# Performance work log

Measured on AMD Instinct MI355X. Metric: run time of the kernel, lower is better.

The kernel has to match this reference:

```python
import jax, jax.numpy as jnp
import numpy as np

ROI_SIZE = 7
MAX_BIN_H = 8   # max adaptive-maxpool bin height for crop H <= 37
MAX_BIN_W = 9   # max adaptive-maxpool bin width  for crop W <= 50
SCALE = 0.0625  # 1/16 feature stride


def setup_inputs() -> dict:
    key = jax.random.key(0)
    ks = jax.random.split(key, 12)
    B, C, h, w = 1, 512, 37, 50          # conv5 feature map of a 600x800 image
    N = 512                               # number of ROIs (proposals)
    n_class = 21
    d_in, d_fc = C * ROI_SIZE * ROI_SIZE, 4096
    x = jax.random.normal(ks[0], (B, C, h, w), dtype=jnp.float32)
    # rois in image coordinates (x1, y1, x2, y2), image is 800x600
    x1 = jax.random.uniform(ks[1], (N,), minval=0.0, maxval=700.0)
    y1 = jax.random.uniform(ks[2], (N,), minval=0.0, maxval=500.0)
    bw = jax.random.uniform(ks[3], (N,), minval=16.0, maxval=400.0)
    bh = jax.random.uniform(ks[4], (N,), minval=16.0, maxval=300.0)
    rois = jnp.stack([x1, y1, jnp.minimum(x1 + bw, 799.0), jnp.minimum(y1 + bh, 599.0)], axis=1).astype(jnp.float32)
    roi_index = jnp.zeros((N,), dtype=jnp.int32)  # single image in batch
    W1 = jax.random.normal(ks[5], (d_in, d_fc), dtype=jnp.float32) * 0.01
    b1 = jnp.zeros((d_fc,), dtype=jnp.float32)
    W2 = jax.random.normal(ks[6], (d_fc, d_fc), dtype=jnp.float32) * 0.01
    b2 = jnp.zeros((d_fc,), dtype=jnp.float32)
    Wp = jax.random.normal(ks[7], (d_fc, n_class * 4), dtype=jnp.float32) * 0.001
    bp = jax.random.normal(ks[8], (n_class * 4,), dtype=jnp.float32) * 0.001
    Ws = jax.random.normal(ks[9], (d_fc, n_class), dtype=jnp.float32) * 0.01
    bs = jax.random.normal(ks[10], (n_class,), dtype=jnp.float32) * 0.01
    return dict(x=x, rois=rois, roi_index=roi_index, W1=W1, b1=b1, W2=W2, b2=b2, Wp=Wp, bp=bp, Ws=Ws, bs=bs)


def _roi_pool(x, rois, roi_index):
    """Faithful port of roi_pooling(): per-ROI crop + AdaptiveMaxPool2d(7)."""
    B, C, h, w = x.shape
    S = ROI_SIZE
    coords = jnp.round(rois * SCALE)  # round-half-even, like torch.round
    cx1 = jnp.clip(coords[:, 0], 0, w).astype(jnp.int32)
    cy1 = jnp.clip(coords[:, 1], 0, h).astype(jnp.int32)
    cx2 = jnp.clip(coords[:, 2], 0, w).astype(jnp.int32)
    cy2 = jnp.clip(coords[:, 3], 0, h).astype(jnp.int32)
    bidx = roi_index.astype(jnp.int32)
    roi_stack = jnp.stack([bidx, cx1, cy1, cx2, cy2], axis=1)  # [N,5]

    def pool_one(carry, roi):
        bi, x1i, y1i, x2i, y2i = roi[0], roi[1], roi[2], roi[3], roi[4]
        valid = (x1i < x2i) & (y1i < y2i)
        # torch slicing roi[2]:roi[4]+1 silently truncates at the tensor edge
        x2e = jnp.minimum(x2i, w - 1)
        y2e = jnp.minimum(y2i, h - 1)
        Hc = y2e - y1i + 1
        Wc = x2e - x1i + 1
        i = jnp.arange(S)
        # adaptive max pool bins: [floor(i*H/S), ceil((i+1)*H/S))
        rs = y1i + (i * Hc) // S
        re = y1i + ((i + 1) * Hc + S - 1) // S
        cs = x1i + (i * Wc) // S
        ce = x1i + ((i + 1) * Wc + S - 1) // S
        rows = rs[:, None] + jnp.arange(MAX_BIN_H)          # [S, MBH]
        rmask = rows < re[:, None]
        rows = jnp.clip(rows, 0, h - 1)
        cols = cs[:, None] + jnp.arange(MAX_BIN_W)          # [S, MBW]
        cmask = cols < ce[:, None]
        cols = jnp.clip(cols, 0, w - 1)
        feat = x[bi]                                         # [C, h, w]
        g = feat[:, rows[:, None, :, None], cols[None, :, None, :]]  # [C,S,S,MBH,MBW]
        mask = rmask[:, None, :, None] & cmask[None, :, None, :]     # [S,S,MBH,MBW]
        pooled = jnp.where(mask, g, -jnp.inf).max(axis=(-2, -1))    # [C,S,S]
        pooled = jnp.where(valid, pooled, jnp.zeros_like(pooled))
        return carry, pooled

    _, out = jax.lax.scan(pool_one, None, roi_stack)  # [N, C, S, S]
    return out


def reference(x, rois, roi_index, W1, b1, W2, b2, Wp, bp, Ws, bs):
    pooled = _roi_pool(x, rois, roi_index)            # [N, 512, 7, 7]
    flat = pooled.reshape(pooled.shape[0], -1)        # [N, 25088]
    fc6 = jax.nn.relu(flat @ W1 + b1)                 # [N, 4096]
    fc7 = jax.nn.relu(fc6 @ W2 + b2)                  # [N, 4096]
    roi_class_params = fc7 @ Wp + bp                  # [N, n_class*4]
    roi_scores = fc7 @ Ws + bs                        # [N, n_class]
    return (roi_class_params, roi_scores)
```

## Files before the change

### kernel.cpp

```cpp
#include <hip/hip_runtime.h>
#include <hip/hip_bf16.h>

using f32x4  = float          __attribute__((ext_vector_type(4)));
using bf16x8 = __bf16         __attribute__((ext_vector_type(8)));
using u16x8  = unsigned short __attribute__((ext_vector_type(8)));

#define C_CH 512
#define H_IN 37
#define W_IN 50
#define NPOS 1850
#define NROI 512
#define DIN  25088
#define DFC  4096
#define NPAR 84
#define NCLS 21
#define KS1   4
#define KS2   8
#define KSH   8

#define PB_X  232
#define PB_WH 2048
#define PB_TOT (PB_X + PB_WH)

__device__ __forceinline__ unsigned pack_bf16x2(float a, float b) {
    __hip_bfloat162 h;
    h.x = __float2bfloat16(a);
    h.y = __float2bfloat16(b);
    return *reinterpret_cast<unsigned*>(&h);
}

__global__ __launch_bounds__(256) void prep_kernel(
        const float* __restrict__ x, float* __restrict__ xt,
        const float* __restrict__ Wp, const float* __restrict__ Ws,
        float* __restrict__ Whp) {
    __shared__ float tile[64][65];
    int b = blockIdx.x;
    int t = threadIdx.x;
    if (b < PB_X) {
        int p0 = (b % 29) * 64;
        int c0 = (b / 29) * 64;
        int tc = t & 63, tr = t >> 6;
#pragma unroll
        for (int i = 0; i < 16; ++i) {
            int r = tr + i * 4;
            int p = p0 + tc;
            float v = 0.f;
            if (p < NPOS) v = x[(size_t)(c0 + r) * NPOS + p];
            tile[r][tc] = v;
        }
        __syncthreads();
#pragma unroll
        for (int i = 0; i < 16; ++i) {
            int rw = tr + i * 4;
            int p = p0 + rw;
            if (p < NPOS) xt[(size_t)p * C_CH + c0 + tc] = tile[tc][rw];
        }
    } else {
        int idx = (b - PB_X) * 256 + t;
        int k = idx >> 7, c = idx & 127;
        float v = 0.f;
        if (c < NPAR) v = Wp[(size_t)k * NPAR + c];
        else if (c < NPAR + NCLS) v = Ws[(size_t)k * NCLS + (c - NPAR)];
        Whp[idx] = v;
    }
}

__global__ __launch_bounds__(256) void roi_pool_kernel(
        const float* __restrict__ xt, const float* __restrict__ rois,
        __hip_bfloat16* __restrict__ pooled) {
    int n = blockIdx.x;
    int t = threadIdx.x;
    float4 rv = reinterpret_cast<const float4*>(rois)[n];
    int x1 = (int)fminf(fmaxf(rintf(rv.x * 0.0625f), 0.f), (float)W_IN);
    int y1 = (int)fminf(fmaxf(rintf(rv.y * 0.0625f), 0.f), (float)H_IN);
    int x2 = (int)fminf(fmaxf(rintf(rv.z * 0.0625f), 0.f), (float)W_IN);
    int y2 = (int)fminf(fmaxf(rintf(rv.w * 0.0625f), 0.f), (float)H_IN);
    bool valid = (x1 < x2) && (y1 < y2);
    unsigned* outp = reinterpret_cast<unsigned*>(pooled) + (size_t)n * (DIN / 2);
    if (!valid) {
        for (int b = 0; b < 49; ++b) outp[b * 256 + t] = 0u;
        return;
    }
    int x2e = min(x2, W_IN - 1), y2e = min(y2, H_IN - 1);
    int Hc = y2e - y1 + 1, Wc = x2e - x1 + 1;
    const float2* base = reinterpret_cast<const float2*>(xt);
    for (int i = 0; i < 7; ++i) {
        int rs = y1 + (i * Hc) / 7;
        int re = y1 + ((i + 1) * Hc + 6) / 7;
        for (int j = 0; j < 7; ++j) {
            int cs = x1 + (j * Wc) / 7;
            int ce = x1 + ((j + 1) * Wc + 6) / 7;
            float m0 = -__builtin_inff(), m1 = -__builtin_inff();
            for (int r = rs; r < re; ++r) {
                const float2* rowp = base + (size_t)r * (W_IN * C_CH / 2) + t;
                for (int c = cs; c < ce; ++c) {
                    float2 v = rowp[c * (C_CH / 2)];
                    m0 = fmaxf(m0, v.x);
                    m1 = fmaxf(m1, v.y);
                }
            }
            outp[(i * 7 + j) * 256 + t] = pack_bf16x2(m0, m1);
        }
    }
}

__device__ __forceinline__ void gload_lds16(const void* src, void* dst) {
    __builtin_amdgcn_global_load_lds(
        (const __attribute__((address_space(1))) void*)src,
        (__attribute__((address_space(3))) void*)dst, 16, 0, 0);
}

__global__ __launch_bounds__(256, 2) void gemm_f32b_kernel(
        const __hip_bfloat16* __restrict__ A,
        const float* __restrict__ Bf,
        float* __restrict__ Cp,
        int N, int lda, int ldbn, int kChunk, int nMT, int nNT, int Mtot,
        int perm) {
    __shared__ __align__(16) char lA0[16384];
    __shared__ __align__(16) char lA1[16384];
    __shared__ __align__(16) char lA2[16384];
    __shared__ __align__(16) char lB0[16384];
    __shared__ __align__(16) char lB1[16384];

    int q = gridDim.x >> 3;
    int bid = (blockIdx.x & 7) * q + (blockIdx.x >> 3);
    int mt = bid % nMT;
    int nt = (bid / nMT) % nNT;
    int ks = bid / (nMT * nNT);
    int m0 = mt * 128, n0 = nt * 128;
    int k0 = ks * kChunk;
    int t = threadIdx.x;
    int lane = t & 63, wid = t >> 6;

    const char* srcA[4]; int offA[4];
#pragma unroll
    for (int i = 0; i < 4; ++i) {
        int chunk = i * 4 + wid;
        int p = chunk * 1024 + lane * 16;
        int row = p >> 7;
        int swz = ((row ^ (row >> 3)) & 7) << 4;
        srcA[i] = (const char*)A + ((size_t)(m0 + row) * lda + k0) * 2
                  + ((p & 127) ^ swz);
        offA[i] = chunk * 1024;
    }
    auto stageA = [&](char* buf) {
#pragma unroll
        for (int i = 0; i < 4; ++i) {
            gload_lds16(srcA[i], buf + offA[i]);
            srcA[i] += 128;
        }
    };

    int n4 = (t & 31) * 4;
    int k8 = (t >> 5) * 8;
    int rstr = perm ? 49 : 1;
    const float* pB = Bf + n0 + n4;
    int koff[8];
#pragma unroll
    for (int p = 0; p < 8; ++p) koff[p] = (k8 + p) * rstr * ldbn;
    int woff[4];
#pragma unroll
    for (int j = 0; j < 4; ++j) {
        int row = n4 + j;
        int swz = ((row ^ (row >> 3)) & 7) << 4;
        woff[j] = row * 128 + ((k8 * 2) ^ swz);
    }
    auto loadB = [&](int kt, f32x4 (&v)[8]) {
        int kb = k0 + (kt << 6);
        int rb = perm ? ((kb & 511) * 49 + (kb >> 9)) : kb;
        int rbo = rb * ldbn;
#pragma unroll
        for (int p = 0; p < 8; ++p)
            v[p] = *reinterpret_cast<const f32x4*>(pB + (size_t)(rbo + koff[p]));
    };
    auto cvtB = [&](f32x4 (&v)[8], char* bW) {
#pragma unroll
        for (int j = 0; j < 4; ++j) {
            uint4 w;
            w.x = pack_bf16x2(v[0][j], v[1][j]);
            w.y = pack_bf16x2(v[2][j], v[3][j]);
            w.z = pack_bf16x2(v[4][j], v[5][j]);
            w.w = pack_bf16x2(v[6][j], v[7][j]);
            *reinterpret_cast<uint4*>(bW + woff[j]) = w;
        }
    };

    int wm = wid >> 1, wn = wid & 1;
    int kb0 = (lane >> 4) << 4;
    int roA[4], roB[4], sA[4], sB[4];
#pragma unroll
    for (int f = 0; f < 4; ++f) {
        int ra = wm * 64 + f * 16 + (lane & 15);
        int rb = wn * 64 + f * 16 + (lane & 15);
        roA[f] = ra * 128; sA[f] = ((ra ^ (ra >> 3)) & 7) << 4;
        roB[f] = rb * 128; sB[f] = ((rb ^ (rb >> 3)) & 7) << 4;
    }

    f32x4 acc[4][4] = {};
    auto mfmaStep = [&](const char* bA, const char* bB) {
        __builtin_amdgcn_s_setprio(1);
#pragma unroll
        for (int ksub = 0; ksub < 2; ++ksub) {
            int kk = kb0 | (ksub << 6);
            bf16x8 af[4], bfr[4];
#pragma unroll
            for (int f = 0; f < 4; ++f)
                af[f] = *reinterpret_cast<const bf16x8*>(bA + roA[f] + (kk ^ sA[f]));
#pragma unroll
            for (int f = 0; f < 4; ++f)
                bfr[f] = *reinterpret_cast<const bf16x8*>(bB + roB[f] + (kk ^ sB[f]));
#pragma unroll
            for (int mf = 0; mf < 4; ++mf)
#pragma unroll
                for (int nf = 0; nf < 4; ++nf)
                    acc[mf][nf] = __builtin_amdgcn_mfma_f32_16x16x32_bf16(
                        af[mf], bfr[nf], acc[mf][nf], 0, 0, 0);
        }
        __builtin_amdgcn_s_setprio(0);
    };

    f32x4 sP[8], sQ[8];
    auto body = [&](int kt, char* aR, char* aS,
                    f32x4 (&vC)[8], f32x4 (&vL)[8], char* bR, char* bW) {
        stageA(aS);
        loadB(kt + 2, vL);
        mfmaStep(aR, bR);
        cvtB(vC, bW);
        asm volatile("s_waitcnt lgkmcnt(0)\ns_barrier" ::: "memory");
    };

    int nkt = kChunk >> 6;

    stageA(lA0);
    stageA(lA1);
    loadB(0, sP);
    loadB(1, sQ);
    cvtB(sP, lB0);
    asm volatile("s_waitcnt lgkmcnt(0)\ns_barrier" ::: "memory");

    for (int kt = 0; kt + 2 < nkt; kt += 6) {
        body(kt + 0, lA0, lA2, sQ, sP, lB0, lB1);
        body(kt + 1, lA1, lA0, sP, sQ, lB1, lB0);
        body(kt + 2, lA2, lA1, sQ, sP, lB0, lB1);
        body(kt + 3, lA0, lA2, sP, sQ, lB1, lB0);
        body(kt + 4, lA1, lA0, sQ, sP, lB0, lB1);
        body(kt + 5, lA2, lA1, sP, sQ, lB1, lB0);
    }
    mfmaStep(lA0, lB0);
    cvtB(sQ, lB1);
    asm volatile("s_waitcnt vmcnt(0) lgkmcnt(0)\ns_barrier" ::: "memory");
    mfmaStep(lA1, lB1);

    float* outp = Cp + (size_t)ks * Mtot * N;
    int rbase = m0 + wm * 64;
    int cbase = n0 + wn * 64 + (lane & 15);
    int rl = (lane >> 4) * 4;
#pragma unroll
    for (int mf = 0; mf < 4; ++mf)
#pragma unroll
        for (int nf = 0; nf < 4; ++nf)
#pragma unroll
            for (int r = 0; r < 4; ++r)
                outp[(size_t)(rbase + mf * 16 + rl + r) * N + cbase + nf * 16] =
                    acc[mf][nf][r];
}

__global__ __launch_bounds__(256) void reduce_bias_relu_kernel(
        const float* __restrict__ P, const float* __restrict__ bias,
        __hip_bfloat16* __restrict__ out, int MN, int N, int KS) {
    int idx = blockIdx.x * blockDim.x + threadIdx.x;
    int e0 = idx * 4;
    if (e0 >= MN) return;
    f32x4 s = *reinterpret_cast<const f32x4*>(P + e0);
    for (int k = 1; k < KS; ++k)
        s += *reinterpret_cast<const f32x4*>(P + (size_t)k * MN + e0);
    f32x4 b = *reinterpret_cast<const f32x4*>(bias + (e0 & (N - 1)));
    s += b;
    uint2 pk;
    pk.x = pack_bf16x2(fmaxf(s[0], 0.f), fmaxf(s[1], 0.f));
    pk.y = pack_bf16x2(fmaxf(s[2], 0.f), fmaxf(s[3], 0.f));
    *reinterpret_cast<uint2*>(reinterpret_cast<char*>(out) + (size_t)e0 * 2) = pk;
}

__global__ __launch_bounds__(128) void head_reduce_kernel(
        const float* __restrict__ P, const float* __restrict__ bp,
        const float* __restrict__ bs, float* __restrict__ out, int KS) {
    int n = blockIdx.x, c = threadIdx.x;
    float s = 0.f;
    for (int ks = 0; ks < KS; ++ks)
        s += P[(size_t)ks * NROI * 128 + (size_t)n * 128 + c];
    if (c < NPAR)
        out[(size_t)n * NPAR + c] = s + bp[c];
    else if (c < NPAR + NCLS)
        out[(size_t)NROI * NPAR + (size_t)n * NCLS + (c - NPAR)] = s + bs[c - NPAR];
}

extern "C" void kernel_launch(void* const* d_in, const int* in_sizes, int n_in,
                              void* d_out, int out_size, void* d_ws, size_t ws_size,
                              hipStream_t stream) {
    const float* x    = (const float*)d_in[0];
    const float* rois = (const float*)d_in[1];
    const float* W1 = (const float*)d_in[3];
    const float* b1 = (const float*)d_in[4];
    const float* W2 = (const float*)d_in[5];
    const float* b2 = (const float*)d_in[6];
    const float* Wp = (const float*)d_in[7];
    const float* bp = (const float*)d_in[8];
    const float* Ws = (const float*)d_in[9];
    const float* bs = (const float*)d_in[10];
    float* out = (float*)d_out;

    const size_t MB = 1ull << 20;
    char* ws = (char*)d_ws;
    float*          xt     = (float*)(ws + 0);
    __hip_bfloat16* pooled = (__hip_bfloat16*)(ws + 4   * MB);
    float*          Whp    = (float*)(ws + 30  * MB);
    float*          part   = (float*)(ws + 34  * MB);
    __hip_bfloat16* fc6    = (__hip_bfloat16*)(ws + 104 * MB);
    __hip_bfloat16* fc7    = (__hip_bfloat16*)(ws + 109 * MB);

    prep_kernel<<<PB_TOT, 256, 0, stream>>>(x, xt, Wp, Ws, Whp);
    roi_pool_kernel<<<NROI, 256, 0, stream>>>(xt, rois, pooled);

    gemm_f32b_kernel<<<4 * 32 * KS1, 256, 0, stream>>>(
        pooled, W1, part, DFC, DIN, DFC, DIN / KS1, 4, 32, NROI, 1);
    reduce_bias_relu_kernel<<<2048, 256, 0, stream>>>(part, b1, fc6,
                                                      NROI * DFC, DFC, KS1);

    gemm_f32b_kernel<<<4 * 32 * KS2, 256, 0, stream>>>(
        fc6, W2, part, DFC, DFC, DFC, DFC / KS2, 4, 32, NROI, 0);
    reduce_bias_relu_kernel<<<2048, 256, 0, stream>>>(part, b2, fc7,
                                                      NROI * DFC, DFC, KS2);

    gemm_f32b_kernel<<<4 * KSH, 256, 0, stream>>>(fc7, Whp, part,
                                                  128, DFC, 128, DFC / KSH,
                                                  4, 1, NROI, 0);
    head_reduce_kernel<<<NROI, 128, 0, stream>>>(part, bp, bs, out, KSH);
}
```

Before: 410.6 us.

## Add 256x256-tile GEMM kernel with 512 threads for fc6/fc7 layers

Adds a new GEMM kernel that computes 256x256 output tiles with 8 waves and double-buffered LDS for A (loaded directly via global_load_lds) and B (fp32 converted to bf16 in registers). It replaces the 128x128-tile kernel for the two large FC layers, and the fc6 split-K factor goes from 4 to 8 to keep enough blocks in flight. Larger tiles halve the global re-reads of the fp32 weights and of the activations per FLOP. The cost is larger partial-sum traffic for fc6, a different pipeline depth, and fewer blocks per CU. The setprio calls are also removed from the old kernel, which still handles the head GEMM.

```diff
diff --git a/kernel.cpp b/kernel.cpp
--- a/kernel.cpp
+++ b/kernel.cpp
@@ -14,9 +14,9 @@
 #define DFC  4096
 #define NPAR 84
 #define NCLS 21
-#define KS1   4
-#define KS2   8
-#define KSH   8
+#define KS1  8
+#define KS2  8
+#define KSH  8
 
 #define PB_X  232
 #define PB_WH 2048
@@ -27,6 +27,12 @@
     h.x = __float2bfloat16(a);
     h.y = __float2bfloat16(b);
     return *reinterpret_cast<unsigned*>(&h);
+}
+
+__device__ __forceinline__ void gload_lds16(const void* src, void* dst) {
+    __builtin_amdgcn_global_load_lds(
+        (const __attribute__((address_space(1))) void*)src,
+        (__attribute__((address_space(3))) void*)dst, 16, 0, 0);
 }
 
 __global__ __launch_bounds__(256) void prep_kernel(
@@ -104,10 +110,162 @@
     }
 }
 
-__device__ __forceinline__ void gload_lds16(const void* src, void* dst) {
-    __builtin_amdgcn_global_load_lds(
-        (const __attribute__((address_space(1))) void*)src,
-        (__attribute__((address_space(3))) void*)dst, 16, 0, 0);
+__global__ __launch_bounds__(512, 2) void gemm256_kernel(
+        const __hip_bfloat16* __restrict__ A,
+        const float* __restrict__ Bf,
+        float* __restrict__ Cp,
+        int N, int lda, int ldbn, int kChunk, int nMT, int nNT, int Mtot,
+        int perm) {
+    __shared__ __align__(16) char lA0[32768];
+    __shared__ __align__(16) char lA1[32768];
+    __shared__ __align__(16) char lB0[32768];
+    __shared__ __align__(16) char lB1[32768];
+
+    int q8 = gridDim.x >> 3;
+    int bid = (blockIdx.x & 7) * q8 + (blockIdx.x >> 3);
+    int mt = bid % nMT;
+    int rr = bid / nMT;
+    int nt = rr % nNT;
+    int ks = rr / nNT;
+    int m0 = mt * 256, n0 = nt * 256;
+    int k0 = ks * kChunk;
+    int t = threadIdx.x;
+    int lane = t & 63, wid = t >> 6;
+    int wm = wid >> 2, wn = wid & 3;
+
+    int row0 = wid * 8 + (lane >> 3);
+    int col0 = (lane & 7) * 16;
+    int sw0  = ((row0 ^ (row0 >> 3)) & 7) << 4;
+    const char* srcA0 = (const char*)A + ((size_t)(m0 + row0) * lda + k0) * 2
+                        + (col0 ^ sw0);
+    size_t aIstep = (size_t)64 * lda * 2;
+    int dst0 = wid * 1024 + lane * 16;
+    auto stageA = [&](char* buf, int tau) {
+        const char* s = srcA0 + (size_t)tau * 128;
+#pragma unroll
+        for (int i = 0; i < 4; ++i)
+            gload_lds16(s + (size_t)i * aIstep, buf + dst0 + i * 8192);
+    };
+
+    int n4 = lane * 4;
+    int rstr = perm ? 49 : 1;
+    const float* pB = Bf + n0 + n4;
+    int kstep = rstr * ldbn;
+    int koff0 = (wid * 8) * kstep;
+    f32x4 v[8];
+    auto loadB = [&](int tau) {
+        int kb = k0 + (tau << 6);
+        int rb = perm ? ((kb & 511) * 49 + (kb >> 9)) : kb;
+        const float* p0 = pB + (size_t)rb * ldbn + koff0;
+#pragma unroll
+        for (int p = 0; p < 8; ++p)
+            v[p] = *reinterpret_cast<const f32x4*>(p0 + (size_t)p * kstep);
+    };
+    int woff[4];
+#pragma unroll
+    for (int j = 0; j < 4; ++j) {
+        int row = n4 + j;
+        woff[j] = row * 128 + ((wid * 16) ^ (((row ^ (row >> 3)) & 7) << 4));
+    }
+    auto cvtB = [&](char* buf) {
+#pragma unroll
+        for (int j = 0; j < 4; ++j) {
+            uint4 w;
+            w.x = pack_bf16x2(v[0][j], v[1][j]);
+            w.y = pack_bf16x2(v[2][j], v[3][j]);
+            w.z = pack_bf16x2(v[4][j], v[5][j]);
+            w.w = pack_bf16x2(v[6][j], v[7][j]);
+            *reinterpret_cast<uint4*>(buf + woff[j]) = w;
+        }
+    };
+
+    int kb0 = (lane >> 4) << 4;
+    int pA[8], pBfr[4];
+#pragma unroll
+    for (int f = 0; f < 8; ++f) {
+        int r = wm * 128 + f * 16 + (lane & 15);
+        pA[f] = r * 128 + (((r ^ (r >> 3)) & 7) << 4);
+    }
+#pragma unroll
+    for (int f = 0; f < 4; ++f) {
+        int r = wn * 64 + f * 16 + (lane & 15);
+        pBfr[f] = r * 128 + (((r ^ (r >> 3)) & 7) << 4);
+    }
+
+    f32x4 acc[8][4] = {};
+    bf16x8 bfr[4];
+    auto phase = [&](const char* bufA, const char* bufB, int q, int ksub,
+                     bool ldBf) {
+        int kk = kb0 | (ksub << 6);
+        if (ldBf) {
+#pragma unroll
+            for (int f = 0; f < 4; ++f)
+                bfr[f] = *reinterpret_cast<const bf16x8*>(bufB + (pBfr[f] ^ kk));
+        }
+        bf16x8 af[4];
+#pragma unroll
+        for (int f = 0; f < 4; ++f)
+            af[f] = *reinterpret_cast<const bf16x8*>(bufA + (pA[q * 4 + f] ^ kk));
+        __builtin_amdgcn_s_setprio(1);
+#pragma unroll
+        for (int f = 0; f < 4; ++f)
+#pragma unroll
+            for (int nf = 0; nf < 4; ++nf)
+                acc[q * 4 + f][nf] = __builtin_amdgcn_mfma_f32_16x16x32_bf16(
+                    af[f], bfr[nf], acc[q * 4 + f][nf], 0, 0, 0);
+        __builtin_amdgcn_s_setprio(0);
+        __builtin_amdgcn_sched_barrier(0);
+    };
+
+    int nkt = kChunk >> 6;
+
+    stageA(lA0, 0);
+    stageA(lA1, 1);
+    loadB(0); cvtB(lB0);
+    loadB(1); cvtB(lB1);
+    loadB(2);
+    asm volatile("s_waitcnt vmcnt(8) lgkmcnt(0)" ::: "memory");
+    __builtin_amdgcn_s_barrier();
+
+    int nIter = nkt >> 1;
+    for (int i = 0; i < nIter; ++i) {
+        int ta = 2 * i;
+        phase(lA0, lB0, 0, 0, true);
+        phase(lA0, lB0, 1, 0, false);
+        phase(lA0, lB0, 0, 1, true);
+        phase(lA0, lB0, 1, 1, false);
+        asm volatile("s_waitcnt vmcnt(0) lgkmcnt(0)" ::: "memory");
+        __builtin_amdgcn_s_barrier();
+        if (ta + 2 < nkt) { cvtB(lB0); stageA(lA0, ta + 2); }
+        if (ta + 3 < nkt) loadB(ta + 3);
+        phase(lA1, lB1, 0, 0, true);
+        phase(lA1, lB1, 1, 0, false);
+        phase(lA1, lB1, 0, 1, true);
+        phase(lA1, lB1, 1, 1, false);
+        asm volatile("s_waitcnt vmcnt(0) lgkmcnt(0)" ::: "memory");
+        __builtin_amdgcn_s_barrier();
+        if (ta + 3 < nkt) { cvtB(lB1); stageA(lA1, ta + 3); }
+        if (ta + 4 < nkt) loadB(ta + 4);
+    }
+    if (nkt & 1) {
+        phase(lA0, lB0, 0, 0, true);
+        phase(lA0, lB0, 1, 0, false);
+        phase(lA0, lB0, 0, 1, true);
+        phase(lA0, lB0, 1, 1, false);
+    }
+
+    float* outp = Cp + (size_t)ks * Mtot * N;
+    int rb0 = m0 + wm * 128;
+    int cb = n0 + wn * 64 + (lane & 15);
+    int rl = (lane >> 4) * 4;
+#pragma unroll
+    for (int mf = 0; mf < 8; ++mf)
+#pragma unroll
+        for (int nf = 0; nf < 4; ++nf)
+#pragma unroll
+            for (int r = 0; r < 4; ++r)
+                outp[(size_t)(rb0 + mf * 16 + rl + r) * N + cb + nf * 16] =
+                    acc[mf][nf][r];
 }
 
 __global__ __launch_bounds__(256, 2) void gemm_f32b_kernel(
@@ -198,7 +356,6 @@
 
     f32x4 acc[4][4] = {};
     auto mfmaStep = [&](const char* bA, const char* bB) {
-        __builtin_amdgcn_s_setprio(1);
 #pragma unroll
         for (int ksub = 0; ksub < 2; ++ksub) {
             int kk = kb0 | (ksub << 6);
@@ -216,7 +373,6 @@
                     acc[mf][nf] = __builtin_amdgcn_mfma_f32_16x16x32_bf16(
                         af[mf], bfr[nf], acc[mf][nf], 0, 0, 0);
         }
-        __builtin_amdgcn_s_setprio(0);
     };
 
     f32x4 sP[8], sQ[8];
@@ -322,13 +478,13 @@
     prep_kernel<<<PB_TOT, 256, 0, stream>>>(x, xt, Wp, Ws, Whp);
     roi_pool_kernel<<<NROI, 256, 0, stream>>>(xt, rois, pooled);
 
-    gemm_f32b_kernel<<<4 * 32 * KS1, 256, 0, stream>>>(
-        pooled, W1, part, DFC, DIN, DFC, DIN / KS1, 4, 32, NROI, 1);
+    gemm256_kernel<<<2 * 16 * KS1, 512, 0, stream>>>(
+        pooled, W1, part, DFC, DIN, DFC, DIN / KS1, 2, 16, NROI, 1);
     reduce_bias_relu_kernel<<<2048, 256, 0, stream>>>(part, b1, fc6,
                                                       NROI * DFC, DFC, KS1);
 
-    gemm_f32b_kernel<<<4 * 32 * KS2, 256, 0, stream>>>(
-        fc6, W2, part, DFC, DFC, DFC, DFC / KS2, 4, 32, NROI, 0);
+    gemm256_kernel<<<2 * 16 * KS2, 512, 0, stream>>>(
+        fc6, W2, part, DFC, DFC, DFC, DFC / KS2, 2, 16, NROI, 0);
     reduce_bias_relu_kernel<<<2048, 256, 0, stream>>>(part, b2, fc7,
                                                       NROI * DFC, DFC, KS2);
 
```

Result: slower. 534.4 us (+30.1%).

## Deepen GEMM B prefetch and interleave conversion with MFMA halves

Applied to the files above, without the earlier changes.

Restructures the GEMM main loop so B global loads are issued three tiles ahead instead of two. The bf16 conversion and LDS write of B is placed between the two MFMA k-halves, and A staging is issued after the MFMAs. A partial vmcnt wait replaces the full drain, and the split-K factor for the second FC layer drops from 8 to 4, halving partial-sum traffic at the cost of fewer blocks. The loop is meant to hide global-load latency better, but it now runs per-tile bounds checks and relies on exact vmcnt counts being correct.

```diff
diff --git a/kernel.cpp b/kernel.cpp
--- a/kernel.cpp
+++ b/kernel.cpp
@@ -14,9 +14,9 @@
 #define DFC  4096
 #define NPAR 84
 #define NCLS 21
-#define KS1   4
-#define KS2   8
-#define KSH   8
+#define KS1  4
+#define KS2  4
+#define KSH  8
 
 #define PB_X  232
 #define PB_WH 2048
@@ -27,6 +27,12 @@
     h.x = __float2bfloat16(a);
     h.y = __float2bfloat16(b);
     return *reinterpret_cast<unsigned*>(&h);
+}
+
+__device__ __forceinline__ void gload_lds16(const void* src, void* dst) {
+    __builtin_amdgcn_global_load_lds(
+        (const __attribute__((address_space(1))) void*)src,
+        (__attribute__((address_space(3))) void*)dst, 16, 0, 0);
 }
 
 __global__ __launch_bounds__(256) void prep_kernel(
@@ -104,23 +110,14 @@
     }
 }
 
-__device__ __forceinline__ void gload_lds16(const void* src, void* dst) {
-    __builtin_amdgcn_global_load_lds(
-        (const __attribute__((address_space(1))) void*)src,
-        (__attribute__((address_space(3))) void*)dst, 16, 0, 0);
-}
-
 __global__ __launch_bounds__(256, 2) void gemm_f32b_kernel(
         const __hip_bfloat16* __restrict__ A,
         const float* __restrict__ Bf,
         float* __restrict__ Cp,
         int N, int lda, int ldbn, int kChunk, int nMT, int nNT, int Mtot,
         int perm) {
-    __shared__ __align__(16) char lA0[16384];
-    __shared__ __align__(16) char lA1[16384];
-    __shared__ __align__(16) char lA2[16384];
-    __shared__ __align__(16) char lB0[16384];
-    __shared__ __align__(16) char lB1[16384];
+    __shared__ __align__(16) char lA[3 * 16384];
+    __shared__ __align__(16) char lB[2 * 16384];
 
     int q = gridDim.x >> 3;
     int bid = (blockIdx.x & 7) * q + (blockIdx.x >> 3);
@@ -143,10 +140,10 @@
                   + ((p & 127) ^ swz);
         offA[i] = chunk * 1024;
     }
-    auto stageA = [&](char* buf) {
+    auto stageA = [&](char* slot) {
 #pragma unroll
         for (int i = 0; i < 4; ++i) {
-            gload_lds16(srcA[i], buf + offA[i]);
+            gload_lds16(srcA[i], slot + offA[i]);
             srcA[i] += 128;
         }
     };
@@ -197,59 +194,58 @@
     }
 
     f32x4 acc[4][4] = {};
-    auto mfmaStep = [&](const char* bA, const char* bB) {
-        __builtin_amdgcn_s_setprio(1);
-#pragma unroll
-        for (int ksub = 0; ksub < 2; ++ksub) {
-            int kk = kb0 | (ksub << 6);
-            bf16x8 af[4], bfr[4];
-#pragma unroll
-            for (int f = 0; f < 4; ++f)
-                af[f] = *reinterpret_cast<const bf16x8*>(bA + roA[f] + (kk ^ sA[f]));
-#pragma unroll
-            for (int f = 0; f < 4; ++f)
-                bfr[f] = *reinterpret_cast<const bf16x8*>(bB + roB[f] + (kk ^ sB[f]));
-#pragma unroll
-            for (int mf = 0; mf < 4; ++mf)
-#pragma unroll
-                for (int nf = 0; nf < 4; ++nf)
-                    acc[mf][nf] = __builtin_amdgcn_mfma_f32_16x16x32_bf16(
-                        af[mf], bfr[nf], acc[mf][nf], 0, 0, 0);
-        }
-        __builtin_amdgcn_s_setprio(0);
-    };
-
-    f32x4 sP[8], sQ[8];
-    auto body = [&](int kt, char* aR, char* aS,
-                    f32x4 (&vC)[8], f32x4 (&vL)[8], char* bR, char* bW) {
-        stageA(aS);
-        loadB(kt + 2, vL);
-        mfmaStep(aR, bR);
-        cvtB(vC, bW);
-        asm volatile("s_waitcnt lgkmcnt(0)\ns_barrier" ::: "memory");
+    auto mfmaHalf = [&](const char* bA, const char* bB, int ksub) {
+        int kk = kb0 | (ksub << 6);
+        bf16x8 af[4], bfr[4];
+#pragma unroll
+        for (int f = 0; f < 4; ++f)
+            af[f] = *reinterpret_cast<const bf16x8*>(bA + roA[f] + (kk ^ sA[f]));
+#pragma unroll
+        for (int f = 0; f < 4; ++f)
+            bfr[f] = *reinterpret_cast<const bf16x8*>(bB + roB[f] + (kk ^ sB[f]));
+#pragma unroll
+        for (int mf = 0; mf < 4; ++mf)
+#pragma unroll
+            for (int nf = 0; nf < 4; ++nf)
+                acc[mf][nf] = __builtin_amdgcn_mfma_f32_16x16x32_bf16(
+                    af[mf], bfr[nf], acc[mf][nf], 0, 0, 0);
     };
 
     int nkt = kChunk >> 6;
 
-    stageA(lA0);
-    stageA(lA1);
-    loadB(0, sP);
-    loadB(1, sQ);
-    cvtB(sP, lB0);
-    asm volatile("s_waitcnt lgkmcnt(0)\ns_barrier" ::: "memory");
-
-    for (int kt = 0; kt + 2 < nkt; kt += 6) {
-        body(kt + 0, lA0, lA2, sQ, sP, lB0, lB1);
-        body(kt + 1, lA1, lA0, sP, sQ, lB1, lB0);
-        body(kt + 2, lA2, lA1, sQ, sP, lB0, lB1);
-        body(kt + 3, lA0, lA2, sP, sQ, lB1, lB0);
-        body(kt + 4, lA1, lA0, sQ, sP, lB0, lB1);
-        body(kt + 5, lA2, lA1, sP, sQ, lB1, lB0);
-    }
-    mfmaStep(lA0, lB0);
-    cvtB(sQ, lB1);
-    asm volatile("s_waitcnt vmcnt(0) lgkmcnt(0)\ns_barrier" ::: "memory");
-    mfmaStep(lA1, lB1);
+    f32x4 vP[8], vQ[8];
+    auto body = [&](int tt, char* aR, char* aS,
+                    f32x4 (&vC)[8], char* bR, char* bW) {
+        mfmaHalf(aR, bR, 0);
+        if (tt + 1 < nkt) cvtB(vC, bW);
+        mfmaHalf(aR, bR, 1);
+        if (tt + 2 < nkt) stageA(aS);
+        if (tt + 3 < nkt) {
+            loadB(tt + 3, vC);
+            asm volatile("s_waitcnt vmcnt(12) lgkmcnt(0)\ns_barrier" ::: "memory");
+        } else {
+            asm volatile("s_waitcnt vmcnt(0) lgkmcnt(0)\ns_barrier" ::: "memory");
+        }
+    };
+
+    stageA(lA);
+    stageA(lA + 16384);
+    loadB(0, vP);
+    loadB(1, vQ);
+    cvtB(vP, lB);
+    loadB(2, vP);
+    asm volatile("s_waitcnt vmcnt(12) lgkmcnt(0)\ns_barrier" ::: "memory");
+
+    char* s0 = lA;  char* s1 = lA + 16384;  char* s2 = lA + 32768;
+    char* b0 = lB;  char* b1 = lB + 16384;
+    for (int kt = 0; kt < nkt; kt += 6) {
+        body(kt + 0, s0, s2, vQ, b0, b1);
+        if (kt + 1 < nkt) body(kt + 1, s1, s0, vP, b1, b0);
+        if (kt + 2 < nkt) body(kt + 2, s2, s1, vQ, b0, b1);
+        if (kt + 3 < nkt) body(kt + 3, s0, s2, vP, b1, b0);
+        if (kt + 4 < nkt) body(kt + 4, s1, s0, vQ, b0, b1);
+        if (kt + 5 < nkt) body(kt + 5, s2, s1, vP, b1, b0);
+    }
 
     float* outp = Cp + (size_t)ks * Mtot * N;
     int rbase = m0 + wm * 64;
```

New measurement: 392.0 us. 1.05x faster.
